# Optimization experiments

Measured on AMD Instinct MI355X. Metric: run time of the kernel, lower is better.

The kernel has to match this reference:

```python
import jax, jax.numpy as jnp
import numpy as np

N_NODES = 100000
N_REL = 8
N_EDGES = 100000  # per relation
DIM = 128


def setup_inputs() -> dict:
    key = jax.random.key(0)
    ks = jax.random.split(key, 8)
    s = 1.0 / np.sqrt(DIM)
    return {
        "entity_embeddings": jax.random.normal(ks[0], (N_NODES, DIM), jnp.float32),
        "edge_index": jax.random.randint(ks[1], (N_REL, 2, N_EDGES), 0, N_NODES, jnp.int32),
        "edge_weights": jax.random.uniform(ks[2], (N_REL, N_EDGES), jnp.float32),
        "relW1": jax.random.normal(ks[3], (N_REL, DIM, DIM), jnp.float32) * s,
        "selfW1": jax.random.normal(ks[4], (DIM, DIM), jnp.float32) * s,
        "bias1": jnp.zeros((N_REL, DIM), jnp.float32),
        "relW2": jax.random.normal(ks[5], (N_REL, DIM, DIM), jnp.float32) * s,
        "selfW2": jax.random.normal(ks[6], (DIM, DIM), jnp.float32) * s,
        "bias2": jnp.zeros((N_REL, DIM), jnp.float32),
    }


def _wrgcn_layer(x, edge_index, edge_weights, relW, selfW, bias):
    # x: [N, Din]; edge_index: [R, 2, E]; edge_weights: [R, E]
    N = x.shape[0]
    R, _, E = edge_index.shape
    src = edge_index[:, 0]  # [R, E]
    tgt = edge_index[:, 1]  # [R, E]
    # gather -> per-relation matmul -> edge-weight scale
    src_emb = x[src]  # [R, E, Din]
    msg = jnp.einsum('red,rdo->reo', src_emb, relW) * edge_weights[..., None]  # [R, E, Dout]
    # scatter-add to target nodes (shared node space across relations)
    agg = jax.ops.segment_sum(msg.reshape(R * E, -1), tgt.reshape(R * E), num_segments=N)
    # bias added once per (relation, unique target node)
    tgt_mask = jnp.zeros((R, N), x.dtype).at[jnp.arange(R)[:, None], tgt].set(1.0)  # [R, N]
    agg = agg + jnp.einsum('rn,ro->no', tgt_mask, bias)
    # self loop
    return agg + x @ selfW


def reference(entity_embeddings, edge_index, edge_weights,
              relW1, selfW1, bias1, relW2, selfW2, bias2):
    h = _wrgcn_layer(entity_embeddings, edge_index, edge_weights, relW1, selfW1, bias1)
    h = jax.nn.relu(h)  # dropout is identity in eval mode
    out = _wrgcn_layer(h, edge_index, edge_weights, relW2, selfW2, bias2)
    return out
```

## Files before the change

kernel.cpp:

```cpp
#include <hip/hip_runtime.h>
#include <hip/hip_bf16.h>

#define NN 100000
#define DD 128
#define RR 8
#define EE 100000
#define NP1 (NN + 1)
#define NB1 98
#define PADN (NB1 * 1024)
#define SEG 8
#define WPR (NN / SEG)

typedef __attribute__((ext_vector_type(8))) short short8;
typedef __attribute__((ext_vector_type(4))) float f32x4;

__device__ __forceinline__ unsigned short f2bf(float v) {
  union { float f; unsigned int u; } x; x.f = v;
  unsigned int r = (x.u + 0x7FFFu + ((x.u >> 16) & 1u)) >> 16;
  return (unsigned short)r;
}

__global__ void k_cast4(const float* __restrict__ src, unsigned short* __restrict__ dst, int n4) {
  int i = blockIdx.x * blockDim.x + threadIdx.x;
  int stride = gridDim.x * blockDim.x;
  for (; i < n4; i += stride) {
    float4 v = reinterpret_cast<const float4*>(src)[i];
    ushort4 o;
    o.x = f2bf(v.x); o.y = f2bf(v.y); o.z = f2bf(v.z); o.w = f2bf(v.w);
    reinterpret_cast<ushort4*>(dst)[i] = o;
  }
}

__global__ void k_castT(const float* __restrict__ src, unsigned short* __restrict__ dst, int total) {
  int i = blockIdx.x * blockDim.x + threadIdx.x;
  if (i >= total) return;
  int r = i >> 14;
  int k = (i >> 7) & 127;
  int o = i & 127;
  dst[(r << 14) + (o << 7) + k] = f2bf(src[i]);
}

__global__ void k_zero(unsigned int* __restrict__ p, int n) {
  int i = blockIdx.x * blockDim.x + threadIdx.x;
  if (i < n) p[i] = 0u;
}

__global__ void k_maskbits(const int* __restrict__ edge_index, unsigned int* __restrict__ mb) {
  int e = blockIdx.x * blockDim.x + threadIdx.x;
  int r = blockIdx.y;
  if (e >= EE) return;
  int tgt = edge_index[(size_t)r * 2 * EE + EE + e];
  atomicOr(&mb[tgt], 1u << r);
}


__global__ void k_hist(const int* __restrict__ edge_index, int* __restrict__ cnt) {
  int e = blockIdx.x * blockDim.x + threadIdx.x;
  int r = blockIdx.y;
  if (e >= EE) return;
  int tgt = edge_index[(size_t)r * 2 * EE + EE + e];
  atomicAdd(&cnt[r * PADN + tgt], 1);
}

__global__ void k_scan1(const int* __restrict__ cnt, int* __restrict__ start, int* __restrict__ bsum) {
  const int r = blockIdx.y, b = blockIdx.x, t = threadIdx.x;
  const int bin0 = b * 1024 + t * 4;
  int4 c = *reinterpret_cast<const int4*>(&cnt[r * PADN + bin0]);
  int s1 = c.x, s2 = s1 + c.y, s3 = s2 + c.z, tot = s3 + c.w;
  __shared__ int sh[256];
  sh[t] = tot;
  __syncthreads();
  for (int off = 1; off < 256; off <<= 1) {
    int v = (t >= off) ? sh[t - off] : 0;
    __syncthreads();
    sh[t] += v;
    __syncthreads();
  }
  int excl = sh[t] - tot;
  if (t == 255) bsum[r * NB1 + b] = sh[255];
  const int base = r * NP1;
  if (bin0 < NN) start[base + bin0] = excl;
  if (bin0 + 1 < NN) start[base + bin0 + 1] = excl + s1;
  if (bin0 + 2 < NN) start[base + bin0 + 2] = excl + s2;
  if (bin0 + 3 < NN) start[base + bin0 + 3] = excl + s3;
}

__global__ void k_scan2(const int* __restrict__ bsum, int* __restrict__ boff, int* __restrict__ start) {
  const int r = blockIdx.x, t = threadIdx.x;
  int v = (t < NB1) ? bsum[r * NB1 + t] : 0;
  __shared__ int sh[128];
  sh[t] = v;
  __syncthreads();
  for (int off = 1; off < 128; off <<= 1) {
    int u = (t >= off) ? sh[t - off] : 0;
    __syncthreads();
    sh[t] += u;
    __syncthreads();
  }
  if (t < NB1) boff[r * NB1 + t] = sh[t] - v;
  if (t == 0) start[r * NP1 + NN] = EE;
}

__global__ void k_scan3(int* __restrict__ start, const int* __restrict__ boff, int* __restrict__ cursor) {
  const int r = blockIdx.y, b = blockIdx.x, t = threadIdx.x;
  const int bin0 = b * 1024 + t * 4;
  const int off = boff[r * NB1 + b];
  const int base = r * NP1;
#pragma unroll
  for (int k = 0; k < 4; ++k) {
    int bin = bin0 + k;
    if (bin < NN) {
      int v = start[base + bin] + off;
      start[base + bin] = v;
      cursor[r * NN + bin] = v;
    }
  }
}

__global__ void k_scatter2(const int* __restrict__ edge_index, const float* __restrict__ ew,
                           int* __restrict__ cursor, int2* __restrict__ es) {
  int e = blockIdx.x * blockDim.x + threadIdx.x;
  int r = blockIdx.y;
  if (e >= EE) return;
  const int* src_p = edge_index + (size_t)r * 2 * EE;
  int tgt = src_p[EE + e];
  int pos = atomicAdd(&cursor[r * NN + tgt], 1);
  es[(size_t)r * EE + pos] = make_int2(src_p[e], __float_as_int(ew[(size_t)r * EE + e]));
}


__device__ __forceinline__ void preagg_wave(const unsigned short* __restrict__ Xsrc,
                                            const int2* __restrict__ es,
                                            const int* __restrict__ start,
                                            int r, int n0, int lane,
                                            float (&a0)[SEG], float (&a1)[SEG]) {
  const size_t rEE = (size_t)r * EE;
  int b = start[r * NP1 + n0 + (lane < 8 ? lane : 8)];
  int p[SEG], q[SEG];
#pragma unroll
  for (int i = 0; i < SEG; ++i) { p[i] = __shfl(b, i); q[i] = __shfl(b, i + 1); }
  int rounds = 0;
#pragma unroll
  for (int i = 0; i < SEG; ++i) rounds = max(rounds, q[i] - p[i]);
#pragma unroll
  for (int i = 0; i < SEG; ++i) { a0[i] = 0.f; a1[i] = 0.f; }
  const unsigned int* Xu = reinterpret_cast<const unsigned int*>(Xsrc);
  for (int j = 0; j < rounds; ++j) {
    bool act[SEG]; int srcv[SEG]; float wv[SEG];
#pragma unroll
    for (int i = 0; i < SEG; ++i) {
      int pos = p[i] + j;
      act[i] = pos < q[i];
      int2 e = es[rEE + (act[i] ? pos : 0)];
      srcv[i] = e.x;
      wv[i] = __int_as_float(e.y);
    }
    unsigned int d[SEG];
#pragma unroll
    for (int i = 0; i < SEG; ++i)
      d[i] = act[i] ? Xu[(size_t)srcv[i] * 64 + lane] : 0u;
#pragma unroll
    for (int i = 0; i < SEG; ++i) {
      if (act[i]) {
        union { unsigned int u; float f; } lo, hi;
        lo.u = d[i] << 16;
        hi.u = d[i] & 0xFFFF0000u;
        a0[i] += wv[i] * lo.f;
        a1[i] += wv[i] * hi.f;
      }
    }
  }
}

__launch_bounds__(256, 4)
__global__ void k_preagg_seg3(const unsigned short* __restrict__ Xsrc,
                              const int2* __restrict__ es, const int* __restrict__ start,
                              unsigned short* __restrict__ P0, unsigned short* __restrict__ P1,
                              unsigned short* __restrict__ P2,
                              int rbase, int nrel) {
  const int wid = blockIdx.x * 4 + (threadIdx.x >> 6);
  if (wid >= nrel * WPR) return;
  const int lane = threadIdx.x & 63;
  const int rr = wid / WPR;
  const int n0 = (wid - rr * WPR) * SEG;
  float a0[SEG], a1[SEG];
  preagg_wave(Xsrc, es, start, rbase + rr, n0, lane, a0, a1);
  unsigned short* P = (rr == 0) ? P0 : ((rr == 1) ? P1 : P2);
  unsigned int* Pw = reinterpret_cast<unsigned int*>(P);
#pragma unroll
  for (int i = 0; i < SEG; ++i)
    Pw[(size_t)(n0 + i) * 64 + lane] = (unsigned int)f2bf(a0[i]) | ((unsigned int)f2bf(a1[i]) << 16);
}

__launch_bounds__(256, 4)
__global__ void k_preagg_seg8(const unsigned short* __restrict__ Xsrc,
                              const int2* __restrict__ es, const int* __restrict__ start,
                              unsigned short* __restrict__ P0, unsigned short* __restrict__ Pws) {
  const int wid = blockIdx.x * 4 + (threadIdx.x >> 6);
  if (wid >= RR * WPR) return;
  const int lane = threadIdx.x & 63;
  const int rr = wid / WPR;
  const int n0 = (wid - rr * WPR) * SEG;
  float a0[SEG], a1[SEG];
  preagg_wave(Xsrc, es, start, rr, n0, lane, a0, a1);
  unsigned short* P = (rr == 0) ? P0 : (Pws + (size_t)(rr - 1) * NN * DD);
  unsigned int* Pw = reinterpret_cast<unsigned int*>(P);
#pragma unroll
  for (int i = 0; i < SEG; ++i)
    Pw[(size_t)(n0 + i) * 64 + lane] = (unsigned int)f2bf(a0[i]) | ((unsigned int)f2bf(a1[i]) << 16);
}


__device__ __forceinline__ void stage_B(const unsigned short* __restrict__ Wt,
                                        unsigned short* __restrict__ lB, int t) {
#pragma unroll
  for (int c = 0; c < 8; ++c) {
    int g = t + 256 * c;
    int o = g >> 4, kc = g & 15;
    int4 v = *reinterpret_cast<const int4*>(Wt + (o << 7) + (kc << 3));
    *reinterpret_cast<int4*>(&lB[(o << 7) + ((kc ^ (o & 7)) << 3)]) = v;
  }
}

__device__ __forceinline__ void stage_A_gen(const unsigned short* __restrict__ A,
                                            unsigned short* __restrict__ lA, int t, int row0) {
#pragma unroll
  for (int c = 0; c < 8; ++c) {
    int g = t + 256 * c;
    int o = g >> 4, kc = g & 15;
    int grow = row0 + o;
    int sr = grow < NN ? grow : NN - 1;
    int4 v = *reinterpret_cast<const int4*>(A + (size_t)sr * 128 + (kc << 3));
    *reinterpret_cast<int4*>(&lA[(o << 7) + ((kc ^ (o & 7)) << 3)]) = v;
  }
}

__device__ __forceinline__ void mfma_tile(const unsigned short* __restrict__ lA,
                                          const unsigned short* __restrict__ lB,
                                          f32x4 (&acc)[2][8], int w, int l) {
  const int lrow = l & 15, kgrp = l >> 4;
#pragma unroll
  for (int ks = 0; ks < 4; ++ks) {
    int kc = ks * 4 + kgrp;
    int ra = w * 32 + lrow;
    int rb = ra + 16;
    short8 a0 = *reinterpret_cast<const short8*>(&lA[(ra << 7) + ((kc ^ (ra & 7)) << 3)]);
    short8 a1 = *reinterpret_cast<const short8*>(&lA[(rb << 7) + ((kc ^ (rb & 7)) << 3)]);
#pragma unroll
    for (int ct = 0; ct < 8; ++ct) {
      int ro = ct * 16 + lrow;
      short8 b = *reinterpret_cast<const short8*>(&lB[(ro << 7) + ((kc ^ (ro & 7)) << 3)]);
      acc[0][ct] = __builtin_amdgcn_mfma_f32_16x16x32_bf16(a0, b, acc[0][ct], 0, 0, 0);
      acc[1][ct] = __builtin_amdgcn_mfma_f32_16x16x32_bf16(a1, b, acc[1][ct], 0, 0, 0);
    }
  }
}

template <bool L1>
__launch_bounds__(256, 2)
__global__ void k_gemm_fused(const unsigned short* __restrict__ Aself,
                             const unsigned short* __restrict__ Wself,
                             const unsigned short* __restrict__ P0,
                             const unsigned short* __restrict__ Pws,
                             const unsigned short* __restrict__ Wrel,
                             const unsigned int* __restrict__ maskbits,
                             const float* __restrict__ bias,
                             void* __restrict__ outp) {
  __shared__ __align__(16) unsigned short lA[128 * 128];
  __shared__ __align__(16) unsigned short lB[128 * 128];
  const int t = threadIdx.x;
  const int row0 = blockIdx.x * 128;
  const int w = t >> 6, l = t & 63;
  const int lrow = l & 15, kgrp = l >> 4;
  f32x4 acc[2][8] = {};

  stage_A_gen(Aself, lA, t, row0);
  stage_B(Wself, lB, t);
  __syncthreads();
  mfma_tile(lA, lB, acc, w, l);
#pragma unroll 1
  for (int r = 0; r < RR; ++r) {
    const unsigned short* Pr = (r == 0) ? P0 : (Pws + (size_t)(r - 1) * NN * DD);
    __syncthreads();
    stage_A_gen(Pr, lA, t, row0);
    stage_B(Wrel + (r << 14), lB, t);
    __syncthreads();
    mfma_tile(lA, lB, acc, w, l);
  }

  {
    short8 a0 = {}, a1 = {}, bf[8];
#pragma unroll
    for (int ct = 0; ct < 8; ++ct) bf[ct] = short8{};
    if (kgrp == 0) {
      int ra = row0 + w * 32 + lrow;
      int rb = ra + 16;
      unsigned int ma = (ra < NN) ? maskbits[ra] : 0u;
      unsigned int mb = (rb < NN) ? maskbits[rb] : 0u;
#pragma unroll
      for (int k = 0; k < 8; ++k) {
        a0[k] = (short)(((ma >> k) & 1u) ? 0x3F80 : 0);
        a1[k] = (short)(((mb >> k) & 1u) ? 0x3F80 : 0);
      }
#pragma unroll
      for (int ct = 0; ct < 8; ++ct) {
        int o = ct * 16 + lrow;
#pragma unroll
        for (int k = 0; k < 8; ++k) bf[ct][k] = (short)f2bf(bias[k * 128 + o]);
      }
    }
#pragma unroll
    for (int ct = 0; ct < 8; ++ct) {
      acc[0][ct] = __builtin_amdgcn_mfma_f32_16x16x32_bf16(a0, bf[ct], acc[0][ct], 0, 0, 0);
      acc[1][ct] = __builtin_amdgcn_mfma_f32_16x16x32_bf16(a1, bf[ct], acc[1][ct], 0, 0, 0);
    }
  }

#pragma unroll
  for (int rt = 0; rt < 2; ++rt) {
#pragma unroll
    for (int j = 0; j < 4; ++j) {
      int grow = row0 + w * 32 + rt * 16 + kgrp * 4 + j;
      if (grow < NN) {
        if (L1) {
          unsigned short* op = (unsigned short*)outp + (size_t)grow * 128 + lrow;
#pragma unroll
          for (int ct = 0; ct < 8; ++ct) op[ct * 16] = f2bf(fmaxf(acc[rt][ct][j], 0.f));
        } else {
          float* op = (float*)outp + (size_t)grow * 128 + lrow;
#pragma unroll
          for (int ct = 0; ct < 8; ++ct) op[ct * 16] = acc[rt][ct][j];
        }
      }
    }
  }
}

template <int NT>
__launch_bounds__(256, 2)
__global__ void k_gemm_multi(const unsigned short* __restrict__ A0, const unsigned short* __restrict__ W0,
                             const unsigned short* __restrict__ A1, const unsigned short* __restrict__ W1,
                             const unsigned short* __restrict__ A2, const unsigned short* __restrict__ W2,
                             const unsigned short* __restrict__ A3, const unsigned short* __restrict__ W3,
                             float* __restrict__ outp, int accum) {
  __shared__ __align__(16) unsigned short lA[128 * 128];
  __shared__ __align__(16) unsigned short lB[128 * 128];
  const int t = threadIdx.x;
  const int row0 = blockIdx.x * 128;
  const int w = t >> 6, l = t & 63;
  const int lrow = l & 15, kgrp = l >> 4;
  f32x4 acc[2][8] = {};

  const unsigned short* As[4] = {A0, A1, A2, A3};
  const unsigned short* Ws[4] = {W0, W1, W2, W3};
#pragma unroll
  for (int term = 0; term < NT; ++term) {
    if (term) __syncthreads();
    stage_A_gen(As[term], lA, t, row0);
    stage_B(Ws[term], lB, t);
    __syncthreads();
    mfma_tile(lA, lB, acc, w, l);
  }

#pragma unroll
  for (int rt = 0; rt < 2; ++rt) {
#pragma unroll
    for (int j = 0; j < 4; ++j) {
      int grow = row0 + w * 32 + rt * 16 + kgrp * 4 + j;
      if (grow < NN) {
        float* op = outp + (size_t)grow * 128 + lrow;
        if (accum) {
#pragma unroll
          for (int ct = 0; ct < 8; ++ct) op[ct * 16] += acc[rt][ct][j];
        } else {
#pragma unroll
          for (int ct = 0; ct < 8; ++ct) op[ct * 16] = acc[rt][ct][j];
        }
      }
    }
  }
}

__global__ void k_epi1(const float* __restrict__ h32, const unsigned int* __restrict__ maskbits,
                       const float* __restrict__ bias, unsigned short* __restrict__ hb) {
  int gid = blockIdx.x * blockDim.x + threadIdx.x;
  if (gid >= NN * 32) return;
  int n = gid >> 5, c = (gid & 31) << 2;
  float4 v = *reinterpret_cast<const float4*>(h32 + (size_t)n * 128 + c);
  unsigned int mb = maskbits[n];
  float b0 = 0, b1 = 0, b2 = 0, b3 = 0;
#pragma unroll
  for (int r = 0; r < RR; ++r) {
    if ((mb >> r) & 1u) {
      const float* bp = bias + r * 128 + c;
      b0 += bp[0]; b1 += bp[1]; b2 += bp[2]; b3 += bp[3];
    }
  }
  ushort4 o;
  o.x = f2bf(fmaxf(v.x + b0, 0.f));
  o.y = f2bf(fmaxf(v.y + b1, 0.f));
  o.z = f2bf(fmaxf(v.z + b2, 0.f));
  o.w = f2bf(fmaxf(v.w + b3, 0.f));
  *reinterpret_cast<ushort4*>(hb + (size_t)n * 128 + c) = o;
}

__global__ void k_epi2(float* __restrict__ out, const unsigned int* __restrict__ maskbits,
                       const float* __restrict__ bias) {
  int gid = blockIdx.x * blockDim.x + threadIdx.x;
  if (gid >= NN * 32) return;
  int n = gid >> 5, c = (gid & 31) << 2;
  unsigned int mb = maskbits[n];
  if (!mb) return;
  float b0 = 0, b1 = 0, b2 = 0, b3 = 0;
#pragma unroll
  for (int r = 0; r < RR; ++r) {
    if ((mb >> r) & 1u) {
      const float* bp = bias + r * 128 + c;
      b0 += bp[0]; b1 += bp[1]; b2 += bp[2]; b3 += bp[3];
    }
  }
  float* p = out + (size_t)n * 128 + c;
  float4 v = *reinterpret_cast<const float4*>(p);
  v.x += b0; v.y += b1; v.z += b2; v.w += b3;
  *reinterpret_cast<float4*>(p) = v;
}

extern "C" void kernel_launch(void* const* d_in, const int* in_sizes, int n_in,
                              void* d_out, int out_size, void* d_ws, size_t ws_size,
                              hipStream_t stream) {
  const float* X   = (const float*)d_in[0];
  const int*   EI  = (const int*)d_in[1];
  const float* EW  = (const float*)d_in[2];
  const float* rW1 = (const float*)d_in[3];
  const float* sW1 = (const float*)d_in[4];
  const float* b1  = (const float*)d_in[5];
  const float* rW2 = (const float*)d_in[6];
  const float* sW2 = (const float*)d_in[7];
  const float* b2  = (const float*)d_in[8];
  float* out = (float*)d_out;
  char* ws = (char*)d_ws;

  size_t off = 0;
  auto take = [&](size_t sz) { char* p = ws + off; off += (sz + 255) & ~(size_t)255; return p; };
  unsigned short* Xb   = (unsigned short*)take((size_t)NN * DD * 2);
  unsigned short* hb   = (unsigned short*)take((size_t)NN * DD * 2);
  unsigned int*  maskb = (unsigned int*)take((size_t)NN * 4);
  unsigned short* rW1t = (unsigned short*)take((size_t)RR * DD * DD * 2);
  unsigned short* sW1t = (unsigned short*)take((size_t)DD * DD * 2);
  unsigned short* rW2t = (unsigned short*)take((size_t)RR * DD * DD * 2);
  unsigned short* sW2t = (unsigned short*)take((size_t)DD * DD * 2);
  int*   cnt    = (int*)take((size_t)RR * PADN * 4);
  int*   start  = (int*)take((size_t)RR * NP1 * 4);
  int*   cursor = (int*)take((size_t)RR * NN * 4);
  int*   bsum   = (int*)take((size_t)RR * NB1 * 4);
  int*   boff   = (int*)take((size_t)RR * NB1 * 4);
  int2*  es     = (int2*)take((size_t)RR * EE * 8);

  const size_t szReg = ((size_t)NN * DD * 2 + 255) & ~(size_t)255;
  const bool bigA = (off + 7 * szReg <= ws_size);
  unsigned short* Pws = nullptr;
  float* h32 = nullptr;
  if (bigA) {
    Pws = (unsigned short*)take(7 * szReg);
  } else {
    h32 = (float*)take((size_t)NN * DD * 4);
  }

  k_cast4<<<2048, 256, 0, stream>>>(X, Xb, NN * DD / 4);
  k_castT<<<(RR * DD * DD + 255) / 256, 256, 0, stream>>>(rW1, rW1t, RR * DD * DD);
  k_castT<<<(DD * DD + 255) / 256, 256, 0, stream>>>(sW1, sW1t, DD * DD);
  k_castT<<<(RR * DD * DD + 255) / 256, 256, 0, stream>>>(rW2, rW2t, RR * DD * DD);
  k_castT<<<(DD * DD + 255) / 256, 256, 0, stream>>>(sW2, sW2t, DD * DD);

  k_zero<<<(NN + 255) / 256, 256, 0, stream>>>(maskb, NN);
  k_maskbits<<<dim3((EE + 255) / 256, RR), 256, 0, stream>>>(EI, maskb);

  k_zero<<<(RR * PADN + 255) / 256, 256, 0, stream>>>((unsigned int*)cnt, RR * PADN);
  k_hist<<<dim3((EE + 255) / 256, RR), 256, 0, stream>>>(EI, cnt);
  k_scan1<<<dim3(NB1, RR), 256, 0, stream>>>(cnt, start, bsum);
  k_scan2<<<RR, 128, 0, stream>>>(bsum, boff, start);
  k_scan3<<<dim3(NB1, RR), 256, 0, stream>>>(start, boff, cursor);
  k_scatter2<<<dim3((EE + 255) / 256, RR), 256, 0, stream>>>(EI, EW, cursor, es);

  const int nblk = (NN + 127) / 128;
  unsigned short* outu = (unsigned short*)d_out;

  if (bigA) {
    const int pblk = (RR * WPR + 3) / 4;
    k_preagg_seg8<<<pblk, 256, 0, stream>>>(Xb, es, start, outu, Pws);
    k_gemm_fused<true><<<nblk, 256, 0, stream>>>(Xb, sW1t, outu, Pws, rW1t, maskb, b1, hb);
    k_preagg_seg8<<<pblk, 256, 0, stream>>>(hb, es, start, Xb, Pws);
    k_gemm_fused<false><<<nblk, 256, 0, stream>>>(hb, sW2t, Xb, Pws, rW2t, maskb, b2, out);
  } else {
    unsigned short* h32u = (unsigned short*)h32;
    const int pblk3 = (3 * WPR + 3) / 4;
    const int pblk2 = (2 * WPR + 3) / 4;
    {
      unsigned short* P0 = outu;
      unsigned short* P1 = outu + (size_t)NN * DD;
      unsigned short* P2 = hb;
      k_preagg_seg3<<<pblk3, 256, 0, stream>>>(Xb, es, start, P0, P1, P2, 0, 3);
      k_gemm_multi<4><<<nblk, 256, 0, stream>>>(Xb, sW1t, P0, rW1t, P1, rW1t + (1 << 14), P2, rW1t + (2 << 14), h32, 0);
      k_preagg_seg3<<<pblk3, 256, 0, stream>>>(Xb, es, start, P0, P1, P2, 3, 3);
      k_gemm_multi<3><<<nblk, 256, 0, stream>>>(P0, rW1t + (3 << 14), P1, rW1t + (4 << 14), P2, rW1t + (5 << 14), nullptr, nullptr, h32, 1);
      k_preagg_seg3<<<pblk2, 256, 0, stream>>>(Xb, es, start, P0, P1, P2, 6, 2);
      k_gemm_multi<2><<<nblk, 256, 0, stream>>>(P0, rW1t + (6 << 14), P1, rW1t + (7 << 14), nullptr, nullptr, nullptr, nullptr, h32, 1);
    }
    k_epi1<<<(NN * 32 + 255) / 256, 256, 0, stream>>>(h32, maskb, b1, hb);
    {
      unsigned short* P0 = h32u;
      unsigned short* P1 = h32u + (size_t)NN * DD;
      unsigned short* P2 = Xb;
      k_preagg_seg3<<<pblk3, 256, 0, stream>>>(hb, es, start, P0, P1, P2, 0, 3);
      k_gemm_multi<4><<<nblk, 256, 0, stream>>>(hb, sW2t, P0, rW2t, P1, rW2t + (1 << 14), P2, rW2t + (2 << 14), out, 0);
      k_preagg_seg3<<<pblk3, 256, 0, stream>>>(hb, es, start, P0, P1, P2, 3, 3);
      k_gemm_multi<3><<<nblk, 256, 0, stream>>>(P0, rW2t + (3 << 14), P1, rW2t + (4 << 14), P2, rW2t + (5 << 14), nullptr, nullptr, out, 1);
      k_preagg_seg3<<<pblk2, 256, 0, stream>>>(hb, es, start, P0, P1, P2, 6, 2);
      k_gemm_multi<2><<<nblk, 256, 0, stream>>>(P0, rW2t + (6 << 14), P1, rW2t + (7 << 14), nullptr, nullptr, nullptr, nullptr, out, 1);
    }
    k_epi2<<<(NN * 32 + 255) / 256, 256, 0, stream>>>(out, maskb, b2);
  }
}
```

Before: 451.2 us.

## Fuse setup kernels and load edge lists cooperatively in pre-aggregation

Merges the four weight-transpose casts into two launches and folds the target mask bitset into the histogram kernel, so there are fewer small launches and one fewer pass over edge targets. In the pre-aggregation wave, a segment of up to 64 edges is now loaded with one coalesced read, one edge per lane, and each source index and weight is broadcast with shuffles. This replaces the per-segment redundant edge loads and adds an early exit for empty segments. The per-segment branches may add divergence, and gather loads are now issued inside the conditional loop, which may reduce memory-level parallelism.

After: 433.0 us. 4.0% less time.

```diff
diff --git a/kernel.cpp b/kernel.cpp
--- a/kernel.cpp
+++ b/kernel.cpp
@@ -31,9 +31,13 @@
   }
 }
 
-__global__ void k_castT(const float* __restrict__ src, unsigned short* __restrict__ dst, int total) {
+__global__ void k_castT2(const float* __restrict__ s1, unsigned short* __restrict__ d1,
+                         const float* __restrict__ s2, unsigned short* __restrict__ d2,
+                         int total) {
   int i = blockIdx.x * blockDim.x + threadIdx.x;
   if (i >= total) return;
+  const float* src = blockIdx.y ? s2 : s1;
+  unsigned short* dst = blockIdx.y ? d2 : d1;
   int r = i >> 14;
   int k = (i >> 7) & 127;
   int o = i & 127;
@@ -45,21 +49,14 @@
   if (i < n) p[i] = 0u;
 }
 
-__global__ void k_maskbits(const int* __restrict__ edge_index, unsigned int* __restrict__ mb) {
-  int e = blockIdx.x * blockDim.x + threadIdx.x;
-  int r = blockIdx.y;
-  if (e >= EE) return;
-  int tgt = edge_index[(size_t)r * 2 * EE + EE + e];
-  atomicOr(&mb[tgt], 1u << r);
-}
-
-
-__global__ void k_hist(const int* __restrict__ edge_index, int* __restrict__ cnt) {
+__global__ void k_hist_mask(const int* __restrict__ edge_index, int* __restrict__ cnt,
+                            unsigned int* __restrict__ mb) {
   int e = blockIdx.x * blockDim.x + threadIdx.x;
   int r = blockIdx.y;
   if (e >= EE) return;
   int tgt = edge_index[(size_t)r * 2 * EE + EE + e];
   atomicAdd(&cnt[r * PADN + tgt], 1);
+  atomicOr(&mb[tgt], 1u << r);
 }
 
 __global__ void k_scan1(const int* __restrict__ cnt, int* __restrict__ start, int* __restrict__ bsum) {
@@ -139,34 +136,53 @@
   int p[SEG], q[SEG];
 #pragma unroll
   for (int i = 0; i < SEG; ++i) { p[i] = __shfl(b, i); q[i] = __shfl(b, i + 1); }
+#pragma unroll
+  for (int i = 0; i < SEG; ++i) { a0[i] = 0.f; a1[i] = 0.f; }
+  const int p0 = p[0];
+  const int count = q[SEG - 1] - p0;
+  if (count <= 0) return;
   int rounds = 0;
 #pragma unroll
   for (int i = 0; i < SEG; ++i) rounds = max(rounds, q[i] - p[i]);
-#pragma unroll
-  for (int i = 0; i < SEG; ++i) { a0[i] = 0.f; a1[i] = 0.f; }
   const unsigned int* Xu = reinterpret_cast<const unsigned int*>(Xsrc);
-  for (int j = 0; j < rounds; ++j) {
-    bool act[SEG]; int srcv[SEG]; float wv[SEG];
-#pragma unroll
-    for (int i = 0; i < SEG; ++i) {
-      int pos = p[i] + j;
-      act[i] = pos < q[i];
-      int2 e = es[rEE + (act[i] ? pos : 0)];
-      srcv[i] = e.x;
-      wv[i] = __int_as_float(e.y);
-    }
-    unsigned int d[SEG];
-#pragma unroll
-    for (int i = 0; i < SEG; ++i)
-      d[i] = act[i] ? Xu[(size_t)srcv[i] * 64 + lane] : 0u;
-#pragma unroll
-    for (int i = 0; i < SEG; ++i) {
-      if (act[i]) {
-        union { unsigned int u; float f; } lo, hi;
-        lo.u = d[i] << 16;
-        hi.u = d[i] & 0xFFFF0000u;
-        a0[i] += wv[i] * lo.f;
-        a1[i] += wv[i] * hi.f;
+
+  if (count <= 64) {
+    int wl = lane < count ? lane : count - 1;
+    int2 ew = es[rEE + p0 + wl];
+    int esrc = ew.x;
+    float ewgt = __int_as_float(ew.y);
+    for (int j = 0; j < rounds; ++j) {
+#pragma unroll
+      for (int i = 0; i < SEG; ++i) {
+        int pos = p[i] + j;
+        if (pos < q[i]) {
+          int widx = pos - p0;
+          int s = __shfl(esrc, widx);
+          float wv = __shfl(ewgt, widx);
+          unsigned int d = Xu[(size_t)s * 64 + lane];
+          union { unsigned int u; float f; } lo, hi;
+          lo.u = d << 16;
+          hi.u = d & 0xFFFF0000u;
+          a0[i] += wv * lo.f;
+          a1[i] += wv * hi.f;
+        }
+      }
+    }
+  } else {
+    for (int j = 0; j < rounds; ++j) {
+#pragma unroll
+      for (int i = 0; i < SEG; ++i) {
+        int pos = p[i] + j;
+        if (pos < q[i]) {
+          int2 e = es[rEE + pos];
+          float wv = __int_as_float(e.y);
+          unsigned int d = Xu[(size_t)e.x * 64 + lane];
+          union { unsigned int u; float f; } lo, hi;
+          lo.u = d << 16;
+          hi.u = d & 0xFFFF0000u;
+          a0[i] += wv * lo.f;
+          a1[i] += wv * hi.f;
+        }
       }
     }
   }
@@ -467,16 +483,12 @@
   }
 
   k_cast4<<<2048, 256, 0, stream>>>(X, Xb, NN * DD / 4);
-  k_castT<<<(RR * DD * DD + 255) / 256, 256, 0, stream>>>(rW1, rW1t, RR * DD * DD);
-  k_castT<<<(DD * DD + 255) / 256, 256, 0, stream>>>(sW1, sW1t, DD * DD);
-  k_castT<<<(RR * DD * DD + 255) / 256, 256, 0, stream>>>(rW2, rW2t, RR * DD * DD);
-  k_castT<<<(DD * DD + 255) / 256, 256, 0, stream>>>(sW2, sW2t, DD * DD);
+  k_castT2<<<dim3((RR * DD * DD + 255) / 256, 2), 256, 0, stream>>>(rW1, rW1t, rW2, rW2t, RR * DD * DD);
+  k_castT2<<<dim3((DD * DD + 255) / 256, 2), 256, 0, stream>>>(sW1, sW1t, sW2, sW2t, DD * DD);
 
   k_zero<<<(NN + 255) / 256, 256, 0, stream>>>(maskb, NN);
-  k_maskbits<<<dim3((EE + 255) / 256, RR), 256, 0, stream>>>(EI, maskb);
-
   k_zero<<<(RR * PADN + 255) / 256, 256, 0, stream>>>((unsigned int*)cnt, RR * PADN);
-  k_hist<<<dim3((EE + 255) / 256, RR), 256, 0, stream>>>(EI, cnt);
+  k_hist_mask<<<dim3((EE + 255) / 256, RR), 256, 0, stream>>>(EI, cnt, maskb);
   k_scan1<<<dim3(NB1, RR), 256, 0, stream>>>(cnt, start, bsum);
   k_scan2<<<RR, 128, 0, stream>>>(bsum, boff, start);
   k_scan3<<<dim3(NB1, RR), 256, 0, stream>>>(start, boff, cursor);
```
